# Performance work log

Measured on AMD Instinct MI355X. Metric: run time of the kernel, lower is better.

Reference implementation:

```python
import jax, jax.numpy as jnp
import numpy as np

N_NODES = 50000
NUM_FEATURES = 128
HIDDEN = 128
OUT = 64
N_EDGES = 600000


def gcn_conv(x, edge_index, W, b, n_nodes):
    """PyG GCNConv: add self-loops, symmetric deg^{-1/2} normalization,
    x' = D^{-1/2}(A+I)D^{-1/2} (x @ W) + b."""
    xw = x @ W  # [N, out]
    loop = jnp.arange(n_nodes, dtype=edge_index.dtype)
    row = jnp.concatenate([edge_index[0], loop])  # source
    col = jnp.concatenate([edge_index[1], loop])  # target
    ones = jnp.ones(row.shape[0], dtype=xw.dtype)
    deg = jax.ops.segment_sum(ones, col, num_segments=n_nodes)  # in-degree incl. self-loop
    dis = jnp.where(deg > 0, jax.lax.rsqrt(deg), 0.0)
    norm = dis[row] * dis[col]  # [E+N]
    msg = xw[row] * norm[:, None]  # gather + scale
    agg = jax.ops.segment_sum(msg, col, num_segments=n_nodes)  # scatter-add
    return agg + b


def setup_inputs() -> dict:
    key = jax.random.key(0)
    ks = jax.random.split(key, 10)
    x = jax.random.normal(ks[0], (N_NODES, NUM_FEATURES), dtype=jnp.float32)
    edge_index = jax.random.randint(ks[1], (2, N_EDGES), 0, N_NODES, dtype=jnp.int64)
    s1 = 1.0 / np.sqrt(NUM_FEATURES)
    s2 = 1.0 / np.sqrt(HIDDEN)
    s3 = 1.0 / np.sqrt(OUT)
    # encoder GCN weights stored as [in, out]
    W_enc1 = jax.random.uniform(ks[2], (NUM_FEATURES, HIDDEN), jnp.float32, -s1, s1)
    b_enc1 = jnp.zeros((HIDDEN,), jnp.float32)
    W_enc2 = jax.random.uniform(ks[3], (HIDDEN, OUT), jnp.float32, -s2, s2)
    b_enc2 = jnp.zeros((OUT,), jnp.float32)
    # decoder Linear weights stored as [in, out]
    W_dec1 = jax.random.uniform(ks[4], (OUT, HIDDEN), jnp.float32, -s3, s3)
    b_dec1 = jax.random.uniform(ks[5], (HIDDEN,), jnp.float32, -s3, s3)
    W_dec2 = jax.random.uniform(ks[6], (HIDDEN, NUM_FEATURES), jnp.float32, -s2, s2)
    b_dec2 = jax.random.uniform(ks[7], (NUM_FEATURES,), jnp.float32, -s2, s2)
    return {"x": x, "edge_index": edge_index,
            "W_enc1": W_enc1, "b_enc1": b_enc1,
            "W_enc2": W_enc2, "b_enc2": b_enc2,
            "W_dec1": W_dec1, "b_dec1": b_dec1,
            "W_dec2": W_dec2, "b_dec2": b_dec2}


def reference(x, edge_index, W_enc1, b_enc1, W_enc2, b_enc2,
              W_dec1, b_dec1, W_dec2, b_dec2):
    n = x.shape[0]
    z = jax.nn.relu(gcn_conv(x, edge_index, W_enc1, b_enc1, n))
    z = jax.nn.relu(gcn_conv(z, edge_index, W_enc2, b_enc2, n))
    z = jax.nn.relu(z @ W_dec1 + b_dec1)
    x_hat = z @ W_dec2 + b_dec2
    return x_hat
```

## Files before the change

kernel.cpp:

```cpp
#include <hip/hip_runtime.h>
#include <hip/hip_bf16.h>


#define N_FEAT 128
#define HID    128
#define OUTD   64

typedef __hip_bfloat16 bf16;
typedef unsigned short u16;
typedef __attribute__((ext_vector_type(8))) short short8;
typedef __attribute__((ext_vector_type(4))) float f32x4;

__device__ __forceinline__ float bs2f(short s) {
    return __builtin_bit_cast(float, ((unsigned)(unsigned short)s) << 16);
}
__device__ __forceinline__ short f2bs(float f) {
    __hip_bfloat16 h = __float2bfloat16(f);
    return __builtin_bit_cast(short, h);
}


__global__ void k_fillslot(const int* __restrict__ row, const int* __restrict__ col,
                           int E, int SL, int npg,
                           int* __restrict__ cnt, u16* __restrict__ slots, int n,
                           const float* __restrict__ W1, const float* __restrict__ W2,
                           const float* __restrict__ Wd1, const float* __restrict__ Wd2,
                           bf16* __restrict__ W1t, bf16* __restrict__ W2t,
                           bf16* __restrict__ Wd1t, bf16* __restrict__ Wd2t) {
    int b = blockIdx.x;
    if (b >= 8 * SL) {
        int i = (b - 8 * SL) * 256 + threadIdx.x;
        if (i < 16384) {
            int k = i >> 7, nn = i & 127;
            W1t[nn * 128 + k] = __float2bfloat16(W1[i]);
        } else if (i < 24576) {
            int j = i - 16384; int k = j >> 6, nn = j & 63;
            W2t[nn * 128 + k] = __float2bfloat16(W2[j]);
        } else if (i < 32768) {
            int j = i - 24576; int k = j >> 7, nn = j & 127;
            Wd1t[nn * 64 + k] = __float2bfloat16(Wd1[j]);
        } else if (i < 49152) {
            int j = i - 32768; int k = j >> 7, nn = j & 127;
            Wd2t[nn * 128 + k] = __float2bfloat16(Wd2[j]);
        }
        return;
    }
    int g = b & 7;
    int s = b >> 3;
    int lo = g * npg;
    int hi = lo + npg; if (hi > n) hi = n;
    int i4 = s * 256 + threadIdx.x;
    int E4 = E >> 2;
    if (i4 < E4) {
        int4 r4 = ((const int4*)row)[i4];
        int4 c4 = ((const int4*)col)[i4];
        int rr[4] = {r4.x, r4.y, r4.z, r4.w};
        int cc[4] = {c4.x, c4.y, c4.z, c4.w};
#pragma unroll
        for (int u = 0; u < 4; ++u) {
            int r = rr[u], c = cc[u];
            if (c >= lo && c < hi && (unsigned)r < (unsigned)n) {
                int pos = atomicAdd(&cnt[c], 1);
                if (pos < 64) slots[(size_t)c * 64 + pos] = (u16)r;
            }
        }
    }
    if (i4 == 0) {
        for (int e = E4 * 4; e < E; ++e) {
            int r = row[e], c = col[e];
            if (c >= lo && c < hi && (unsigned)r < (unsigned)n) {
                int pos = atomicAdd(&cnt[c], 1);
                if (pos < 64) slots[(size_t)c * 64 + pos] = (u16)r;
            }
        }
    }
}


template <int AF32, int OF32, int K, int N>
__global__ void k_gemm(const void* __restrict__ Av, const bf16* __restrict__ Bt,
                       const float* __restrict__ bias,
                       const int* __restrict__ cntp,
                       void* __restrict__ C, int M, int relu) {
    constexpr int KB = K >> 5;
    int t = threadIdx.x;
    int lane = t & 63, w = t >> 6;
    int quad = lane >> 4, l16 = lane & 15;
    int m0 = blockIdx.x * 64 + (w & 1) * 32;
    int nhw = (w >> 1) * 32;
    int kq = quad * 8;

    short8 zero8 = {0, 0, 0, 0, 0, 0, 0, 0};
    int mrow[2]; bool mok[2];
#pragma unroll
    for (int mi = 0; mi < 2; ++mi) {
        mrow[mi] = m0 + mi * 16 + l16;
        mok[mi] = mrow[mi] < M;
    }

    short8 af[2][KB];
#pragma unroll
    for (int mi = 0; mi < 2; ++mi) {
#pragma unroll
        for (int kb = 0; kb < KB; ++kb) {
            if (!mok[mi]) { af[mi][kb] = zero8; continue; }
            int koff = kb * 32 + kq;
            if (AF32) {
                const float* Af = (const float*)Av + (size_t)mrow[mi] * K + koff;
                float4 a = *(const float4*)Af;
                float4 b = *(const float4*)(Af + 4);
                short8 r = {f2bs(a.x), f2bs(a.y), f2bs(a.z), f2bs(a.w),
                            f2bs(b.x), f2bs(b.y), f2bs(b.z), f2bs(b.w)};
                af[mi][kb] = r;
            } else {
                af[mi][kb] = *(const short8*)((const bf16*)Av + (size_t)mrow[mi] * K + koff);
            }
        }
    }

#pragma unroll
    for (int nc = 0; nc < N; nc += 64) {
        int n0 = nc + nhw;
        f32x4 acc[2][2];
#pragma unroll
        for (int mi = 0; mi < 2; ++mi)
#pragma unroll
            for (int ni = 0; ni < 2; ++ni)
#pragma unroll
                for (int r = 0; r < 4; ++r) acc[mi][ni][r] = 0.f;

#pragma unroll
        for (int kb = 0; kb < KB; ++kb) {
            short8 bfm[2];
#pragma unroll
            for (int ni = 0; ni < 2; ++ni) {
                int nn = n0 + ni * 16 + l16;
                bfm[ni] = *(const short8*)(Bt + (size_t)nn * K + kb * 32 + kq);
            }
#pragma unroll
            for (int mi = 0; mi < 2; ++mi)
#pragma unroll
                for (int ni = 0; ni < 2; ++ni)
                    acc[mi][ni] = __builtin_amdgcn_mfma_f32_16x16x32_bf16(
                        af[mi][kb], bfm[ni], acc[mi][ni], 0, 0, 0);
        }

#pragma unroll
        for (int ni = 0; ni < 2; ++ni) {
            int nn = n0 + ni * 16 + l16;
            float bv = bias ? bias[nn] : 0.f;
#pragma unroll
            for (int mi = 0; mi < 2; ++mi) {
#pragma unroll
                for (int r = 0; r < 4; ++r) {
                    int m = m0 + mi * 16 + quad * 4 + r;
                    if (m < M) {
                        float v = acc[mi][ni][r] + bv;
                        if (relu) v = fmaxf(v, 0.f);
                        if (cntp) v *= rsqrtf((float)(cntp[m] + 1));
                        size_t off = (size_t)m * N + nn;
                        if (OF32) ((float*)C)[off] = v;
                        else      ((short*)C)[off] = f2bs(v);
                    }
                }
            }
        }
    }
}


__global__ void k_agg1(const bf16* __restrict__ xw, const int* __restrict__ cnt,
                       const u16* __restrict__ slots,
                       const float* __restrict__ bias, bf16* __restrict__ out,
                       int M) {
    int wv = (int)((blockIdx.x * (size_t)blockDim.x + threadIdx.x) >> 6);
    if (wv >= M) return;
    int lane = threadIdx.x & 63;
    int sub = lane >> 4, li = lane & 15;
    int craw = cnt[wv];
    int cn = min(craw, 64) + 1;
    float dn = rsqrtf((float)(craw + 1));
    const u16* sl = slots + (size_t)wv * 64;

    float a[8] = {0.f, 0.f, 0.f, 0.f, 0.f, 0.f, 0.f, 0.f};
    for (int t = sub; t < cn; t += 16) {
        bool va[4]; short8 v[4];
#pragma unroll
        for (int u = 0; u < 4; ++u) {
            int ti = t + u * 4;
            va[u] = ti < cn;
            int tc = va[u] ? ti : 0;
            int s = (tc == cn - 1) ? wv : (int)sl[tc];
            v[u] = *((const short8*)(xw + (size_t)s * 128) + li);
        }
#pragma unroll
        for (int u = 0; u < 4; ++u)
            if (va[u]) {
#pragma unroll
                for (int j = 0; j < 8; ++j) a[j] += bs2f(v[u][j]);
            }
    }

#pragma unroll
    for (int d = 32; d >= 16; d >>= 1)
#pragma unroll
        for (int j = 0; j < 8; ++j) a[j] += __shfl_down(a[j], d);

    if (lane < 16) {
        float4 b0 = *(const float4*)(bias + lane * 8);
        float4 b1 = *(const float4*)(bias + lane * 8 + 4);
        float bb[8] = {b0.x, b0.y, b0.z, b0.w, b1.x, b1.y, b1.z, b1.w};
        short8 o;
#pragma unroll
        for (int j = 0; j < 8; ++j) o[j] = f2bs(fmaxf(dn * a[j] + bb[j], 0.f));
        *((short8*)(out + (size_t)wv * 128) + lane) = o;
    }
}


__global__ void k_aggdec(const bf16* __restrict__ xw2, const int* __restrict__ cnt,
                         const u16* __restrict__ slots,
                         const float* __restrict__ b2,
                         const bf16* __restrict__ Wd1t, const float* __restrict__ bd1,
                         const bf16* __restrict__ Wd2t, const float* __restrict__ bd2,
                         float* __restrict__ out, int M) {
    __shared__ short h2s[64][72];
    __shared__ short h3s[64][136];
    int t = threadIdx.x;
    int lane = t & 63, w = t >> 6;
    int quad = lane >> 4, l16 = lane & 15;
    int blk = blockIdx.x;

    {
        int sub = lane >> 3;
        int li = lane & 7;
        int sgl = w * 8 + sub;
        int nd0 = blk * 64 + sgl;
        int nd1 = nd0 + 32;
        int cr0 = (nd0 < M) ? cnt[nd0] : -1;
        int cr1 = (nd1 < M) ? cnt[nd1] : -1;
        int cn0 = (nd0 < M) ? min(cr0, 64) + 1 : 0;
        int cn1 = (nd1 < M) ? min(cr1, 64) + 1 : 0;
        const u16* sl0 = slots + (size_t)min(nd0, M - 1) * 64;
        const u16* sl1 = slots + (size_t)min(nd1, M - 1) * 64;

        float a0[8] = {0.f, 0.f, 0.f, 0.f, 0.f, 0.f, 0.f, 0.f};
        float a1[8] = {0.f, 0.f, 0.f, 0.f, 0.f, 0.f, 0.f, 0.f};
        int tmax = cn0 > cn1 ? cn0 : cn1;
        for (int e = 0; e < tmax; e += 4) {
            bool va0[4], va1[4]; short8 v0[4], v1[4];
#pragma unroll
            for (int u = 0; u < 4; ++u) {
                int ei_ = e + u;
                va0[u] = ei_ < cn0;
                int t0 = va0[u] ? ei_ : 0;
                int s0 = (t0 == cn0 - 1) ? nd0 : (int)sl0[t0];
                v0[u] = *((const short8*)(xw2 + (size_t)s0 * 64) + li);
                va1[u] = ei_ < cn1;
                int t1 = va1[u] ? ei_ : 0;
                int s1 = (t1 == cn1 - 1) ? nd1 : (int)sl1[t1];
                v1[u] = *((const short8*)(xw2 + (size_t)s1 * 64) + li);
            }
#pragma unroll
            for (int u = 0; u < 4; ++u) {
                if (va0[u]) {
#pragma unroll
                    for (int j = 0; j < 8; ++j) a0[j] += bs2f(v0[u][j]);
                }
                if (va1[u]) {
#pragma unroll
                    for (int j = 0; j < 8; ++j) a1[j] += bs2f(v1[u][j]);
                }
            }
        }
        float dn0 = (nd0 < M) ? rsqrtf((float)(cr0 + 1)) : 0.f;
        float dn1 = (nd1 < M) ? rsqrtf((float)(cr1 + 1)) : 0.f;
        float4 c0 = *(const float4*)(b2 + li * 8);
        float4 c1 = *(const float4*)(b2 + li * 8 + 4);
        float bb[8] = {c0.x, c0.y, c0.z, c0.w, c1.x, c1.y, c1.z, c1.w};
        short8 o0, o1;
#pragma unroll
        for (int j = 0; j < 8; ++j) {
            o0[j] = f2bs(fmaxf(dn0 * a0[j] + bb[j], 0.f));
            o1[j] = f2bs(fmaxf(dn1 * a1[j] + bb[j], 0.f));
        }
        *(short8*)&h2s[sgl][li * 8] = o0;
        *(short8*)&h2s[sgl + 32][li * 8] = o1;
    }
    __syncthreads();

    int m0 = (w & 1) * 32;
    int nhw = (w >> 1) * 32;
    int kq = quad * 8;

    short8 af1[2][2];
#pragma unroll
    for (int mi = 0; mi < 2; ++mi)
#pragma unroll
        for (int kb = 0; kb < 2; ++kb)
            af1[mi][kb] = *(const short8*)&h2s[m0 + mi * 16 + l16][kb * 32 + kq];

#pragma unroll
    for (int nc = 0; nc < HID; nc += 64) {
        int n0 = nc + nhw;
        f32x4 acc[2][2];
#pragma unroll
        for (int mi = 0; mi < 2; ++mi)
#pragma unroll
            for (int ni = 0; ni < 2; ++ni)
#pragma unroll
                for (int r = 0; r < 4; ++r) acc[mi][ni][r] = 0.f;
#pragma unroll
        for (int kb = 0; kb < 2; ++kb) {
            short8 bfm[2];
#pragma unroll
            for (int ni = 0; ni < 2; ++ni) {
                int nn = n0 + ni * 16 + l16;
                bfm[ni] = *(const short8*)(Wd1t + (size_t)nn * OUTD + kb * 32 + kq);
            }
#pragma unroll
            for (int mi = 0; mi < 2; ++mi)
#pragma unroll
                for (int ni = 0; ni < 2; ++ni)
                    acc[mi][ni] = __builtin_amdgcn_mfma_f32_16x16x32_bf16(
                        af1[mi][kb], bfm[ni], acc[mi][ni], 0, 0, 0);
        }
#pragma unroll
        for (int ni = 0; ni < 2; ++ni) {
            int nn = n0 + ni * 16 + l16;
            float bv = bd1[nn];
#pragma unroll
            for (int mi = 0; mi < 2; ++mi)
#pragma unroll
                for (int r = 0; r < 4; ++r) {
                    int ml = m0 + mi * 16 + quad * 4 + r;
                    h3s[ml][nn] = f2bs(fmaxf(acc[mi][ni][r] + bv, 0.f));
                }
        }
    }
    __syncthreads();

    short8 af2[2][4];
#pragma unroll
    for (int mi = 0; mi < 2; ++mi)
#pragma unroll
        for (int kb = 0; kb < 4; ++kb)
            af2[mi][kb] = *(const short8*)&h3s[m0 + mi * 16 + l16][kb * 32 + kq];

#pragma unroll
    for (int nc = 0; nc < N_FEAT; nc += 64) {
        int n0 = nc + nhw;
        f32x4 acc[2][2];
#pragma unroll
        for (int mi = 0; mi < 2; ++mi)
#pragma unroll
            for (int ni = 0; ni < 2; ++ni)
#pragma unroll
                for (int r = 0; r < 4; ++r) acc[mi][ni][r] = 0.f;
#pragma unroll
        for (int kb = 0; kb < 4; ++kb) {
            short8 bfm[2];
#pragma unroll
            for (int ni = 0; ni < 2; ++ni) {
                int nn = n0 + ni * 16 + l16;
                bfm[ni] = *(const short8*)(Wd2t + (size_t)nn * HID + kb * 32 + kq);
            }
#pragma unroll
            for (int mi = 0; mi < 2; ++mi)
#pragma unroll
                for (int ni = 0; ni < 2; ++ni)
                    acc[mi][ni] = __builtin_amdgcn_mfma_f32_16x16x32_bf16(
                        af2[mi][kb], bfm[ni], acc[mi][ni], 0, 0, 0);
        }
#pragma unroll
        for (int ni = 0; ni < 2; ++ni) {
            int nn = n0 + ni * 16 + l16;
            float bv = bd2[nn];
#pragma unroll
            for (int mi = 0; mi < 2; ++mi)
#pragma unroll
                for (int r = 0; r < 4; ++r) {
                    int m = blk * 64 + m0 + mi * 16 + quad * 4 + r;
                    if (m < M)
                        out[(size_t)m * N_FEAT + nn] = acc[mi][ni][r] + bv;
                }
        }
    }
}


extern "C" void kernel_launch(void* const* d_in, const int* in_sizes, int n_in,
                              void* d_out, int out_size, void* d_ws, size_t ws_size,
                              hipStream_t stream) {
    const float* x   = (const float*)d_in[0];
    const int*   ei  = (const int*)d_in[1];
    const float* W1  = (const float*)d_in[2];
    const float* b1  = (const float*)d_in[3];
    const float* W2  = (const float*)d_in[4];
    const float* b2  = (const float*)d_in[5];
    const float* Wd1 = (const float*)d_in[6];
    const float* bd1 = (const float*)d_in[7];
    const float* Wd2 = (const float*)d_in[8];
    const float* bd2 = (const float*)d_in[9];

    const int n = in_sizes[0] / N_FEAT;
    const int E = in_sizes[1] / 2;
    const int* row = ei;
    const int* col = ei + E;

    char* wp = (char*)d_ws;
    bf16* xw1 = (bf16*)wp;  wp += (size_t)n * 128 * 2;
    bf16* h1  = (bf16*)wp;  wp += (size_t)n * 128 * 2;
    bf16* xw2 = (bf16*)wp;  wp += (size_t)n * 64 * 2;
    bf16* W1t = (bf16*)wp;  wp += 128 * 128 * 2;
    bf16* W2t = (bf16*)wp;  wp += 128 * 64 * 2;
    bf16* Wd1t= (bf16*)wp;  wp += 64 * 128 * 2;
    bf16* Wd2t= (bf16*)wp;  wp += 128 * 128 * 2;
    int* cnt   = (int*)wp;   wp += (size_t)n * 4;
    u16* slots = (u16*)wp;   wp += (size_t)n * 64 * 2;

    hipMemsetAsync(cnt, 0, (size_t)n * sizeof(int), stream);
    int E4 = E >> 2;
    int SL = (E4 + 255) / 256;
    int npg = (n + 7) / 8;
    k_fillslot<<<8 * SL + 192, 256, 0, stream>>>(row, col, E, SL, npg,
                                                 cnt, slots, n,
                                                 W1, W2, Wd1, Wd2,
                                                 W1t, W2t, Wd1t, Wd2t);

    int mg = (n + 63) / 64;
    dim3 blk(256);

    k_gemm<1, 0, 128, 128><<<mg, blk, 0, stream>>>(x, W1t, nullptr, cnt, xw1, n, 0);
    k_agg1<<<(n + 3) / 4, 256, 0, stream>>>(xw1, cnt, slots, b1, h1, n);
    k_gemm<0, 0, 128, 64><<<mg, blk, 0, stream>>>(h1, W2t, nullptr, cnt, xw2, n, 0);
    k_aggdec<<<mg, blk, 0, stream>>>(xw2, cnt, slots, b2,
                                     Wd1t, bd1, Wd2t, bd2, (float*)d_out, n);
}
```

Before: 223.6 us.

## Fuse first GEMM with edge binning and layer-1 aggregation with second GEMM

```diff
diff --git a/kernel.cpp b/kernel.cpp
--- a/kernel.cpp
+++ b/kernel.cpp
@@ -20,33 +20,115 @@
 }
 
 
-__global__ void k_fillslot(const int* __restrict__ row, const int* __restrict__ col,
-                           int E, int SL, int npg,
-                           int* __restrict__ cnt, u16* __restrict__ slots, int n,
-                           const float* __restrict__ W1, const float* __restrict__ W2,
-                           const float* __restrict__ Wd1, const float* __restrict__ Wd2,
-                           bf16* __restrict__ W1t, bf16* __restrict__ W2t,
-                           bf16* __restrict__ Wd1t, bf16* __restrict__ Wd2t) {
+__global__ void k_prep(int* __restrict__ cnt, int n, int ZB,
+                       const float* __restrict__ W1, const float* __restrict__ W2,
+                       const float* __restrict__ Wd1, const float* __restrict__ Wd2,
+                       bf16* __restrict__ W1t, bf16* __restrict__ W2t,
+                       bf16* __restrict__ Wd1t, bf16* __restrict__ Wd2t) {
     int b = blockIdx.x;
-    if (b >= 8 * SL) {
-        int i = (b - 8 * SL) * 256 + threadIdx.x;
-        if (i < 16384) {
-            int k = i >> 7, nn = i & 127;
-            W1t[nn * 128 + k] = __float2bfloat16(W1[i]);
-        } else if (i < 24576) {
-            int j = i - 16384; int k = j >> 6, nn = j & 63;
-            W2t[nn * 128 + k] = __float2bfloat16(W2[j]);
-        } else if (i < 32768) {
-            int j = i - 24576; int k = j >> 7, nn = j & 127;
-            Wd1t[nn * 64 + k] = __float2bfloat16(Wd1[j]);
-        } else if (i < 49152) {
-            int j = i - 32768; int k = j >> 7, nn = j & 127;
-            Wd2t[nn * 128 + k] = __float2bfloat16(Wd2[j]);
-        }
+    if (b < ZB) {
+        int i4 = b * 256 + threadIdx.x;
+        int n4 = n >> 2;
+        if (i4 < n4) ((int4*)cnt)[i4] = make_int4(0, 0, 0, 0);
+        if (i4 == 0) for (int i = n4 * 4; i < n; ++i) cnt[i] = 0;
         return;
     }
-    int g = b & 7;
-    int s = b >> 3;
+    int i = (b - ZB) * 256 + threadIdx.x;
+    if (i < 16384) {
+        int k = i >> 7, nn = i & 127;
+        W1t[nn * 128 + k] = __float2bfloat16(W1[i]);
+    } else if (i < 24576) {
+        int j = i - 16384; int k = j >> 6, nn = j & 63;
+        W2t[nn * 128 + k] = __float2bfloat16(W2[j]);
+    } else if (i < 32768) {
+        int j = i - 24576; int k = j >> 7, nn = j & 127;
+        Wd1t[nn * 64 + k] = __float2bfloat16(Wd1[j]);
+    } else if (i < 49152) {
+        int j = i - 32768; int k = j >> 7, nn = j & 127;
+        Wd2t[nn * 128 + k] = __float2bfloat16(Wd2[j]);
+    }
+}
+
+
+__global__ void k_mega(const int* __restrict__ row, const int* __restrict__ col,
+                       int E, int SL, int npg, int GB,
+                       int* __restrict__ cnt, u16* __restrict__ slots, int n,
+                       const float* __restrict__ x, const bf16* __restrict__ W1t,
+                       bf16* __restrict__ xw1) {
+    int b = blockIdx.x;
+    if (b < GB) {
+        if (b * 64 >= n) return;
+        int t = threadIdx.x;
+        int lane = t & 63, w = t >> 6;
+        int quad = lane >> 4, l16 = lane & 15;
+        int m0 = b * 64 + (w & 1) * 32;
+        int nhw = (w >> 1) * 32;
+        int kq = quad * 8;
+
+        short8 zero8 = {0, 0, 0, 0, 0, 0, 0, 0};
+        int mrow[2]; bool mok[2];
+#pragma unroll
+        for (int mi = 0; mi < 2; ++mi) {
+            mrow[mi] = m0 + mi * 16 + l16;
+            mok[mi] = mrow[mi] < n;
+        }
+        short8 af[2][4];
+#pragma unroll
+        for (int mi = 0; mi < 2; ++mi) {
+#pragma unroll
+            for (int kb = 0; kb < 4; ++kb) {
+                if (!mok[mi]) { af[mi][kb] = zero8; continue; }
+                const float* Af = x + (size_t)mrow[mi] * 128 + kb * 32 + kq;
+                float4 a4 = *(const float4*)Af;
+                float4 b4 = *(const float4*)(Af + 4);
+                short8 r = {f2bs(a4.x), f2bs(a4.y), f2bs(a4.z), f2bs(a4.w),
+                            f2bs(b4.x), f2bs(b4.y), f2bs(b4.z), f2bs(b4.w)};
+                af[mi][kb] = r;
+            }
+        }
+#pragma unroll
+        for (int nc = 0; nc < 128; nc += 64) {
+            int n0 = nc + nhw;
+            f32x4 acc[2][2];
+#pragma unroll
+            for (int mi = 0; mi < 2; ++mi)
+#pragma unroll
+                for (int ni = 0; ni < 2; ++ni)
+#pragma unroll
+                    for (int r = 0; r < 4; ++r) acc[mi][ni][r] = 0.f;
+#pragma unroll
+            for (int kb = 0; kb < 4; ++kb) {
+                short8 bfm[2];
+#pragma unroll
+                for (int ni = 0; ni < 2; ++ni) {
+                    int nn = n0 + ni * 16 + l16;
+                    bfm[ni] = *(const short8*)(W1t + (size_t)nn * 128 + kb * 32 + kq);
+                }
+#pragma unroll
+                for (int mi = 0; mi < 2; ++mi)
+#pragma unroll
+                    for (int ni = 0; ni < 2; ++ni)
+                        acc[mi][ni] = __builtin_amdgcn_mfma_f32_16x16x32_bf16(
+                            af[mi][kb], bfm[ni], acc[mi][ni], 0, 0, 0);
+            }
+#pragma unroll
+            for (int ni = 0; ni < 2; ++ni) {
+                int nn = n0 + ni * 16 + l16;
+#pragma unroll
+                for (int mi = 0; mi < 2; ++mi)
+#pragma unroll
+                    for (int r = 0; r < 4; ++r) {
+                        int m = m0 + mi * 16 + quad * 4 + r;
+                        if (m < n)
+                            ((short*)xw1)[(size_t)m * 128 + nn] = f2bs(acc[mi][ni][r]);
+                    }
+            }
+        }
+        return;
+    }
+    int bb = b - GB;
+    int g = bb & 7;
+    int s = bb >> 3;
     int lo = g * npg;
     int hi = lo + npg; if (hi > n) hi = n;
     int i4 = s * 256 + threadIdx.x;
@@ -77,143 +159,105 @@
 }
 
 
-template <int AF32, int OF32, int K, int N>
-__global__ void k_gemm(const void* __restrict__ Av, const bf16* __restrict__ Bt,
-                       const float* __restrict__ bias,
-                       const int* __restrict__ cntp,
-                       void* __restrict__ C, int M, int relu) {
-    constexpr int KB = K >> 5;
+__global__ void k_aggmm(const bf16* __restrict__ xw1, const int* __restrict__ cnt,
+                        const u16* __restrict__ slots, const float* __restrict__ b1,
+                        const bf16* __restrict__ W2t, bf16* __restrict__ xw2, int M) {
+    __shared__ short h1s[64][136];
     int t = threadIdx.x;
     int lane = t & 63, w = t >> 6;
+    int sub = lane >> 4, li = lane & 15;
+    int blk = blockIdx.x;
+
+    float4 c0 = *(const float4*)(b1 + li * 8);
+    float4 c1 = *(const float4*)(b1 + li * 8 + 4);
+    float bbv[8] = {c0.x, c0.y, c0.z, c0.w, c1.x, c1.y, c1.z, c1.w};
+
+    for (int it = 0; it < 16; ++it) {
+        int nd = blk * 64 + w * 16 + it;
+        bool ok = nd < M;
+        int craw = ok ? cnt[nd] : 0;
+        int cn = ok ? min(craw, 64) + 1 : 0;
+        const u16* sl = slots + (size_t)(ok ? nd : 0) * 64;
+
+        float a[8] = {0.f, 0.f, 0.f, 0.f, 0.f, 0.f, 0.f, 0.f};
+        for (int tt = sub; tt < cn; tt += 16) {
+            bool va[4]; short8 v[4]; float ds[4];
+#pragma unroll
+            for (int u = 0; u < 4; ++u) {
+                int ti = tt + u * 4;
+                va[u] = ti < cn;
+                int tc = va[u] ? ti : 0;
+                int sI = (tc == cn - 1) ? nd : (int)sl[tc];
+                v[u] = *((const short8*)(xw1 + (size_t)sI * 128) + li);
+                ds[u] = rsqrtf((float)(cnt[sI] + 1));
+            }
+#pragma unroll
+            for (int u = 0; u < 4; ++u)
+                if (va[u]) {
+#pragma unroll
+                    for (int j = 0; j < 8; ++j) a[j] += ds[u] * bs2f(v[u][j]);
+                }
+        }
+#pragma unroll
+        for (int d = 32; d >= 16; d >>= 1)
+#pragma unroll
+            for (int j = 0; j < 8; ++j) a[j] += __shfl_down(a[j], d);
+
+        if (lane < 16) {
+            float dn = rsqrtf((float)(craw + 1));
+            short8 o;
+#pragma unroll
+            for (int j = 0; j < 8; ++j) o[j] = f2bs(fmaxf(dn * a[j] + bbv[j], 0.f));
+            *(short8*)&h1s[w * 16 + it][li * 8] = o;
+        }
+    }
+    __syncthreads();
+
     int quad = lane >> 4, l16 = lane & 15;
-    int m0 = blockIdx.x * 64 + (w & 1) * 32;
-    int nhw = (w >> 1) * 32;
-    int kq = quad * 8;
-
-    short8 zero8 = {0, 0, 0, 0, 0, 0, 0, 0};
-    int mrow[2]; bool mok[2];
-#pragma unroll
-    for (int mi = 0; mi < 2; ++mi) {
-        mrow[mi] = m0 + mi * 16 + l16;
-        mok[mi] = mrow[mi] < M;
-    }
-
-    short8 af[2][KB];
-#pragma unroll
-    for (int mi = 0; mi < 2; ++mi) {
-#pragma unroll
-        for (int kb = 0; kb < KB; ++kb) {
-            if (!mok[mi]) { af[mi][kb] = zero8; continue; }
-            int koff = kb * 32 + kq;
-            if (AF32) {
-                const float* Af = (const float*)Av + (size_t)mrow[mi] * K + koff;
-                float4 a = *(const float4*)Af;
-                float4 b = *(const float4*)(Af + 4);
-                short8 r = {f2bs(a.x), f2bs(a.y), f2bs(a.z), f2bs(a.w),
-                            f2bs(b.x), f2bs(b.y), f2bs(b.z), f2bs(b.w)};
-                af[mi][kb] = r;
-            } else {
-                af[mi][kb] = *(const short8*)((const bf16*)Av + (size_t)mrow[mi] * K + koff);
-            }
-        }
-    }
-
-#pragma unroll
-    for (int nc = 0; nc < N; nc += 64) {
-        int n0 = nc + nhw;
-        f32x4 acc[2][2];
+    int m0 = (w & 1) * 32, nhw = (w >> 1) * 32, kq = quad * 8;
+
+    short8 af[2][4];
+#pragma unroll
+    for (int mi = 0; mi < 2; ++mi)
+#pragma unroll
+        for (int kb = 0; kb < 4; ++kb)
+            af[mi][kb] = *(const short8*)&h1s[m0 + mi * 16 + l16][kb * 32 + kq];
+
+    f32x4 acc[2][2];
+#pragma unroll
+    for (int mi = 0; mi < 2; ++mi)
+#pragma unroll
+        for (int ni = 0; ni < 2; ++ni)
+#pragma unroll
+            for (int r = 0; r < 4; ++r) acc[mi][ni][r] = 0.f;
+#pragma unroll
+    for (int kb = 0; kb < 4; ++kb) {
+        short8 bfm[2];
+#pragma unroll
+        for (int ni = 0; ni < 2; ++ni) {
+            int nn = nhw + ni * 16 + l16;
+            bfm[ni] = *(const short8*)(W2t + (size_t)nn * 128 + kb * 32 + kq);
+        }
 #pragma unroll
         for (int mi = 0; mi < 2; ++mi)
 #pragma unroll
             for (int ni = 0; ni < 2; ++ni)
-#pragma unroll
-                for (int r = 0; r < 4; ++r) acc[mi][ni][r] = 0.f;
-
-#pragma unroll
-        for (int kb = 0; kb < KB; ++kb) {
-            short8 bfm[2];
-#pragma unroll
-            for (int ni = 0; ni < 2; ++ni) {
-                int nn = n0 + ni * 16 + l16;
-                bfm[ni] = *(const short8*)(Bt + (size_t)nn * K + kb * 32 + kq);
-            }
-#pragma unroll
-            for (int mi = 0; mi < 2; ++mi)
-#pragma unroll
-                for (int ni = 0; ni < 2; ++ni)
-                    acc[mi][ni] = __builtin_amdgcn_mfma_f32_16x16x32_bf16(
-                        af[mi][kb], bfm[ni], acc[mi][ni], 0, 0, 0);
-        }
-
-#pragma unroll
-        for (int ni = 0; ni < 2; ++ni) {
-            int nn = n0 + ni * 16 + l16;
-            float bv = bias ? bias[nn] : 0.f;
-#pragma unroll
-            for (int mi = 0; mi < 2; ++mi) {
-#pragma unroll
-                for (int r = 0; r < 4; ++r) {
-                    int m = m0 + mi * 16 + quad * 4 + r;
-                    if (m < M) {
-                        float v = acc[mi][ni][r] + bv;
-                        if (relu) v = fmaxf(v, 0.f);
-                        if (cntp) v *= rsqrtf((float)(cntp[m] + 1));
-                        size_t off = (size_t)m * N + nn;
-                        if (OF32) ((float*)C)[off] = v;
-                        else      ((short*)C)[off] = f2bs(v);
-                    }
-                }
-            }
-        }
-    }
-}
-
-
-__global__ void k_agg1(const bf16* __restrict__ xw, const int* __restrict__ cnt,
-                       const u16* __restrict__ slots,
-                       const float* __restrict__ bias, bf16* __restrict__ out,
-                       int M) {
-    int wv = (int)((blockIdx.x * (size_t)blockDim.x + threadIdx.x) >> 6);
-    if (wv >= M) return;
-    int lane = threadIdx.x & 63;
-    int sub = lane >> 4, li = lane & 15;
-    int craw = cnt[wv];
-    int cn = min(craw, 64) + 1;
-    float dn = rsqrtf((float)(craw + 1));
-    const u16* sl = slots + (size_t)wv * 64;
-
-    float a[8] = {0.f, 0.f, 0.f, 0.f, 0.f, 0.f, 0.f, 0.f};
-    for (int t = sub; t < cn; t += 16) {
-        bool va[4]; short8 v[4];
-#pragma unroll
-        for (int u = 0; u < 4; ++u) {
-            int ti = t + u * 4;
-            va[u] = ti < cn;
-            int tc = va[u] ? ti : 0;
-            int s = (tc == cn - 1) ? wv : (int)sl[tc];
-            v[u] = *((const short8*)(xw + (size_t)s * 128) + li);
-        }
-#pragma unroll
-        for (int u = 0; u < 4; ++u)
-            if (va[u]) {
-#pragma unroll
-                for (int j = 0; j < 8; ++j) a[j] += bs2f(v[u][j]);
-            }
-    }
-
-#pragma unroll
-    for (int d = 32; d >= 16; d >>= 1)
-#pragma unroll
-        for (int j = 0; j < 8; ++j) a[j] += __shfl_down(a[j], d);
-
-    if (lane < 16) {
-        float4 b0 = *(const float4*)(bias + lane * 8);
-        float4 b1 = *(const float4*)(bias + lane * 8 + 4);
-        float bb[8] = {b0.x, b0.y, b0.z, b0.w, b1.x, b1.y, b1.z, b1.w};
-        short8 o;
-#pragma unroll
-        for (int j = 0; j < 8; ++j) o[j] = f2bs(fmaxf(dn * a[j] + bb[j], 0.f));
-        *((short8*)(out + (size_t)wv * 128) + lane) = o;
+                acc[mi][ni] = __builtin_amdgcn_mfma_f32_16x16x32_bf16(
+                    af[mi][kb], bfm[ni], acc[mi][ni], 0, 0, 0);
+    }
+#pragma unroll
+    for (int ni = 0; ni < 2; ++ni) {
+        int nn = nhw + ni * 16 + l16;
+#pragma unroll
+        for (int mi = 0; mi < 2; ++mi)
+#pragma unroll
+            for (int r = 0; r < 4; ++r) {
+                int m = blk * 64 + m0 + mi * 16 + quad * 4 + r;
+                if (m < M) {
+                    float v = acc[mi][ni][r] * rsqrtf((float)(cnt[m] + 1));
+                    ((short*)xw2)[(size_t)m * 64 + nn] = f2bs(v);
+                }
+            }
     }
 }
 
@@ -410,7 +454,6 @@
 
     char* wp = (char*)d_ws;
     bf16* xw1 = (bf16*)wp;  wp += (size_t)n * 128 * 2;
-    bf16* h1  = (bf16*)wp;  wp += (size_t)n * 128 * 2;
     bf16* xw2 = (bf16*)wp;  wp += (size_t)n * 64 * 2;
     bf16* W1t = (bf16*)wp;  wp += 128 * 128 * 2;
     bf16* W2t = (bf16*)wp;  wp += 128 * 64 * 2;
@@ -419,21 +462,20 @@
     int* cnt   = (int*)wp;   wp += (size_t)n * 4;
     u16* slots = (u16*)wp;   wp += (size_t)n * 64 * 2;
 
-    hipMemsetAsync(cnt, 0, (size_t)n * sizeof(int), stream);
+    int ZB = (n + 1023) / 1024;
+    k_prep<<<ZB + 192, 256, 0, stream>>>(cnt, n, ZB, W1, W2, Wd1, Wd2,
+                                         W1t, W2t, Wd1t, Wd2t);
+
     int E4 = E >> 2;
     int SL = (E4 + 255) / 256;
     int npg = (n + 7) / 8;
-    k_fillslot<<<8 * SL + 192, 256, 0, stream>>>(row, col, E, SL, npg,
-                                                 cnt, slots, n,
-                                                 W1, W2, Wd1, Wd2,
-                                                 W1t, W2t, Wd1t, Wd2t);
-
     int mg = (n + 63) / 64;
-    dim3 blk(256);
-
-    k_gemm<1, 0, 128, 128><<<mg, blk, 0, stream>>>(x, W1t, nullptr, cnt, xw1, n, 0);
-    k_agg1<<<(n + 3) / 4, 256, 0, stream>>>(xw1, cnt, slots, b1, h1, n);
-    k_gemm<0, 0, 128, 64><<<mg, blk, 0, stream>>>(h1, W2t, nullptr, cnt, xw2, n, 0);
-    k_aggdec<<<mg, blk, 0, stream>>>(xw2, cnt, slots, b2,
+    int GB = (mg + 7) & ~7;
+    k_mega<<<GB + 8 * SL, 256, 0, stream>>>(row, col, E, SL, npg, GB,
+                                            cnt, slots, n, x, W1t, xw1);
+
+    k_aggmm<<<mg, 256, 0, stream>>>(xw1, cnt, slots, b1, W2t, xw2, n);
+
+    k_aggdec<<<mg, 256, 0, stream>>>(xw2, cnt, slots, b2,
                                      Wd1t, bd1, Wd2t, bd2, (float*)d_out, n);
 }
```

New measurement: 213.1 us. -4.7%, faster.
